# Performance work log

Measured on AMD Instinct MI355X. Metric: run time of the kernel, lower is better.

The kernel has to match this reference:

```python
import jax, jax.numpy as jnp
import numpy as np

B, N, S, D, K = 8, 8192, 2048, 256, 3
MLP = [256, 128]
EPS = 1e-5


def setup_inputs() -> dict:
    key = jax.random.key(0)
    ks = jax.random.split(key, 12)
    inp = {
        "xyz1": jax.random.normal(ks[0], (B, N, 3), dtype=jnp.float32),
        "xyz2": jax.random.normal(ks[1], (B, S, 3), dtype=jnp.float32),
        "points1": jax.random.normal(ks[2], (B, N, D), dtype=jnp.float32),
        "points2": jax.random.normal(ks[3], (B, S, D), dtype=jnp.float32),
        # relation conv: Conv2d(4 -> 1, kernel 1x1) == linear over last dim
        "rel_w": jax.random.normal(ks[4], (4,), dtype=jnp.float32) * 0.5,
        "rel_b": jnp.zeros((), dtype=jnp.float32),
        # mlp layer 0: Conv1d(2D -> 256, k=1) + BN
        "W0": jax.random.normal(ks[5], (MLP[0], 2 * D), dtype=jnp.float32) * (1.0 / np.sqrt(2 * D)),
        "b0": jnp.zeros((MLP[0],), dtype=jnp.float32),
        "g0": jnp.ones((MLP[0],), dtype=jnp.float32),
        "be0": jnp.zeros((MLP[0],), dtype=jnp.float32),
        # mlp layer 1: Conv1d(256 -> 128, k=1) + BN
        "W1": jax.random.normal(ks[6], (MLP[1], MLP[0]), dtype=jnp.float32) * (1.0 / np.sqrt(MLP[0])),
        "b1": jnp.zeros((MLP[1],), dtype=jnp.float32),
        "g1": jnp.ones((MLP[1],), dtype=jnp.float32),
        "be1": jnp.zeros((MLP[1],), dtype=jnp.float32),
    }
    return inp


def _gather(points, idx):
    # points: [B,S,C], idx: [B,N,K] -> [B,N,K,C]
    return jax.vmap(lambda p, i: p[i])(points, idx)


def _bn_relu(x, gamma, beta):
    # training-mode BatchNorm1d over [B,N,C]: stats over (B,N), biased var
    mean = jnp.mean(x, axis=(0, 1))
    var = jnp.var(x, axis=(0, 1))
    xn = (x - mean) * jax.lax.rsqrt(var + EPS)
    return jax.nn.relu(xn * gamma + beta)


def reference(xyz1, xyz2, points1, points2, rel_w, rel_b,
              W0, b0, g0, be0, W1, b1, g1, be1):
    # pairwise squared distances [B,N,S]
    d = (jnp.sum(xyz1 ** 2, -1)[:, :, None]
         + jnp.sum(xyz2 ** 2, -1)[:, None, :]
         - 2.0 * jnp.einsum('bnc,bmc->bnm', xyz1, xyz2))
    neg_d, idx = jax.lax.top_k(-d, K)          # K smallest distances
    dists = -neg_d                              # [B,N,K]

    offset = xyz1[:, :, None, :] - _gather(xyz2, idx)        # [B,N,K,3]
    rel = jnp.concatenate([dists[..., None], offset], -1)    # [B,N,K,4]
    weight = jax.nn.sigmoid(rel @ rel_w + rel_b)              # [B,N,K]

    interp = jnp.mean(_gather(points2, idx) * weight[..., None], axis=2)  # [B,N,D]
    h = jnp.concatenate([points1, interp], axis=-1)           # [B,N,2D]

    h = _bn_relu(jnp.einsum('bnc,oc->bno', h, W0) + b0, g0, be0)
    h = _bn_relu(jnp.einsum('bnc,oc->bno', h, W1) + b1, g1, be1)
    return h  # [B,N,128]
```

## Files before the change

kernel.cpp:

```cpp
#include <hip/hip_runtime.h>
#include <stdint.h>
#include <stddef.h>

#define B_   8
#define N_   8192
#define S_   2048
#define D_   256
#define M_   (B_*N_)
#define C0_  256
#define C1_  128
#define K2D_ 512
#define TS8_ 8
#define SEG8_ (S_/TS8_)
#define SWP_ 264

typedef __attribute__((ext_vector_type(8))) short short8;
typedef __attribute__((ext_vector_type(4))) float f32x4;
typedef __attribute__((ext_vector_type(2))) float f32x2;

__device__ __forceinline__ short f2bf(float f) {
  unsigned u = __float_as_uint(f);
  u += 0x7fffu + ((u >> 16) & 1u);
  return (short)(u >> 16);
}
__device__ __forceinline__ float bf2f(short s) {
  return __uint_as_float(((unsigned)(unsigned short)s) << 16);
}

__device__ __forceinline__ void cp16(const void* g, void* l) {
  __builtin_amdgcn_global_load_lds(
      (__attribute__((address_space(1))) void*)(g),
      (__attribute__((address_space(3))) void*)(l), 16, 0, 0);
}

__global__ void convw_kernel(const float* __restrict__ W0,
                             const float* __restrict__ W1,
                             const float* __restrict__ xyz2,
                             short* __restrict__ W0b, short* __restrict__ W1b,
                             float* __restrict__ xyz2p, float* __restrict__ stats) {
  int i = blockIdx.x * 256 + threadIdx.x;
  if (blockIdx.x == 0) {
    stats[threadIdx.x] = 0.f;
    stats[256 + threadIdx.x] = 0.f;
    stats[512 + threadIdx.x] = 0.f;
  }
  if (i < C0_ * K2D_) W0b[i] = f2bf(W0[i]);
  if (i < C1_ * C0_)  W1b[i] = f2bf(W1[i]);
  if (i < B_ * S_) {
    const int b = i >> 11, s = i & (S_ - 1);
    float x = xyz2[(size_t)i * 3 + 0];
    float y = xyz2[(size_t)i * 3 + 1];
    float z = xyz2[(size_t)i * 3 + 2];
    float ss = __fadd_rn(__fadd_rn(__fmul_rn(x, x), __fmul_rn(y, y)), __fmul_rn(z, z));
    float* xw = xyz2p + (size_t)b * 4 * S_;
    xw[s] = x; xw[S_ + s] = y; xw[2 * S_ + s] = z; xw[3 * S_ + s] = ss;
  }
}

__global__ __launch_bounds__(512, 8)
void topk_kernel(const float* __restrict__ xyz1, const float* __restrict__ xyz2p,
                 const float* __restrict__ relw, const float* __restrict__ relb,
                 int* __restrict__ idx_out, float* __restrict__ w_out) {
  __shared__ float cd[TS8_][64][3];
  __shared__ int   ci[TS8_][64][3];
  const int tid  = threadIdx.x;
  const int lane = tid & 63;
  const int seg  = __builtin_amdgcn_readfirstlane(tid >> 6);
  const int b    = blockIdx.x >> 7;
  const int n    = (blockIdx.x & 127) * 64 + lane;

  const float* p = xyz1 + ((size_t)b * N_ + n) * 3;
  const float ax = p[0], ay = p[1], az = p[2];
  const float s1 = __fadd_rn(__fadd_rn(__fmul_rn(ax, ax), __fmul_rn(ay, ay)), __fmul_rn(az, az));

  const float* xw = xyz2p + (size_t)b * 4 * S_;
  const f32x2* XP = (const f32x2*)(xw)           + seg * (SEG8_ / 2);
  const f32x2* YP = (const f32x2*)(xw + S_)      + seg * (SEG8_ / 2);
  const f32x2* ZP = (const f32x2*)(xw + 2 * S_)  + seg * (SEG8_ / 2);
  const f32x2* WP = (const f32x2*)(xw + 3 * S_)  + seg * (SEG8_ / 2);

  float d0 = 3.4e38f, d1 = 3.4e38f, d2 = 3.4e38f;
  int   i0 = 0, i1 = 0, i2 = 0;
  const int sbeg = seg * SEG8_;
  {
    #pragma clang fp contract(off)
    #pragma unroll 4
    for (int pr = 0; pr < SEG8_ / 2; pr++) {
      f32x2 X = XP[pr], Y = YP[pr], Z = ZP[pr], W = WP[pr];
      f32x2 t1 = ax * X;
      f32x2 t2 = ay * Y;
      f32x2 t3 = az * Z;
      f32x2 dt = (t1 + t2) + t3;
      f32x2 e  = s1 + W;
      f32x2 m  = 2.0f * dt;
      f32x2 d  = e - m;
      const float dlo = d.x, dhi = d.y;
      if (fminf(dlo, dhi) < d2) {
        const int s = sbeg + 2 * pr;
        if (dlo < d2) {
          if (dlo < d1) {
            d2 = d1; i2 = i1;
            if (dlo < d0) { d1 = d0; i1 = i0; d0 = dlo; i0 = s; }
            else          { d1 = dlo; i1 = s; }
          } else { d2 = dlo; i2 = s; }
        }
        if (dhi < d2) {
          if (dhi < d1) {
            d2 = d1; i2 = i1;
            if (dhi < d0) { d1 = d0; i1 = i0; d0 = dhi; i0 = s + 1; }
            else          { d1 = dhi; i1 = s + 1; }
          } else { d2 = dhi; i2 = s + 1; }
        }
      }
    }
  }
  cd[seg][lane][0] = d0; cd[seg][lane][1] = d1; cd[seg][lane][2] = d2;
  ci[seg][lane][0] = i0; ci[seg][lane][1] = i1; ci[seg][lane][2] = i2;
  __syncthreads();

  if (tid < 64) {
    float m0 = 3.4e38f, m1 = 3.4e38f, m2 = 3.4e38f;
    int   j0 = 0, j1 = 0, j2 = 0;
    #pragma unroll
    for (int sg = 0; sg < TS8_; sg++) {
      #pragma unroll
      for (int k = 0; k < 3; k++) {
        float d = cd[sg][tid][k];
        int   ix = ci[sg][tid][k];
        if (d < m2) {
          if (d < m1) {
            m2 = m1; j2 = j1;
            if (d < m0) { m1 = m0; j1 = j0; m0 = d; j0 = ix; }
            else        { m1 = d;  j1 = ix; }
          } else { m2 = d; j2 = ix; }
        }
      }
    }
    const float w0r = relw[0], w1r = relw[1], w2r = relw[2], w3r = relw[3], br = relb[0];
    const size_t base = ((size_t)b * N_ + n) * 3;
    float dd[3] = {m0, m1, m2};
    int   ii[3] = {j0, j1, j2};
    #pragma unroll
    for (int k = 0; k < 3; k++) {
      const int s = ii[k];
      float ox = ax - xw[s], oy = ay - xw[S_ + s], oz = az - xw[2 * S_ + s];
      float t = dd[k] * w0r + ox * w1r + oy * w2r + oz * w3r + br;
      float w = 1.0f / (1.0f + expf(-t));
      idx_out[base + k] = s;
      w_out[base + k] = w * (1.0f / 3.0f);
    }
  }
}

__global__ __launch_bounds__(256, 8)
void interp_kernel(const float* __restrict__ p1, const float* __restrict__ p2,
                   const int* __restrict__ idx, const float* __restrict__ wts,
                   short* __restrict__ h) {
  const int tid = threadIdx.x;
  const int seg = tid & 63;
  const size_t row = (size_t)(blockIdx.x & 7) * (M_ / 8)
                   + (size_t)(blockIdx.x >> 3) * 4 + (tid >> 6);
  short8 o;
  if (seg < 32) {
    const float* src = p1 + row * D_ + seg * 8;
    const float4 a = *(const float4*)src;
    const float4 b = *(const float4*)(src + 4);
    o[0] = f2bf(a.x); o[1] = f2bf(a.y); o[2] = f2bf(a.z); o[3] = f2bf(a.w);
    o[4] = f2bf(b.x); o[5] = f2bf(b.y); o[6] = f2bf(b.z); o[7] = f2bf(b.w);
    *(short8*)&h[row * K2D_ + seg * 8] = o;
  } else {
    const int c = (seg - 32) * 8;
    const int i0 = idx[row * 3 + 0], i1 = idx[row * 3 + 1], i2 = idx[row * 3 + 2];
    const float w0 = wts[row * 3 + 0], w1 = wts[row * 3 + 1], w2 = wts[row * 3 + 2];
    const float* pb = p2 + (row >> 13) * ((size_t)S_ * D_) + c;
    const float* q0 = pb + (size_t)i0 * D_;
    const float* q1 = pb + (size_t)i1 * D_;
    const float* q2 = pb + (size_t)i2 * D_;
    const float4 a0 = *(const float4*)q0, b0 = *(const float4*)(q0 + 4);
    const float4 a1 = *(const float4*)q1, b1 = *(const float4*)(q1 + 4);
    const float4 a2 = *(const float4*)q2, b2 = *(const float4*)(q2 + 4);
    float fv[8];
    fv[0] = w0 * a0.x + w1 * a1.x + w2 * a2.x;
    fv[1] = w0 * a0.y + w1 * a1.y + w2 * a2.y;
    fv[2] = w0 * a0.z + w1 * a1.z + w2 * a2.z;
    fv[3] = w0 * a0.w + w1 * a1.w + w2 * a2.w;
    fv[4] = w0 * b0.x + w1 * b1.x + w2 * b2.x;
    fv[5] = w0 * b0.y + w1 * b1.y + w2 * b2.y;
    fv[6] = w0 * b0.z + w1 * b1.z + w2 * b2.z;
    fv[7] = w0 * b0.w + w1 * b1.w + w2 * b2.w;
    #pragma unroll
    for (int e = 0; e < 8; e++) o[e] = f2bf(fv[e]);
    *(short8*)&h[row * K2D_ + D_ + c] = o;
  }
}

__global__ __launch_bounds__(256, 2)
void gemm1_kernel(const short* __restrict__ h, const short* __restrict__ Bw,
                  const float* __restrict__ bias,
                  short* __restrict__ Cb, float* __restrict__ stats) {
  __shared__ __align__(16) short sA[2][128 * 32];
  __shared__ __align__(16) short sB[2][256 * 32];
  const int tid = threadIdx.x;
  const int lane = tid & 63;
  const int wave = tid >> 6;
  const int wm = wave & 1;
  const int wn = wave >> 1;
  const size_t mbase = (size_t)(blockIdx.x & 7) * (M_ / 8)
                     + (size_t)(blockIdx.x >> 3) * 128;

  #define STAGE(K0, BUF)                                                      \
    _Pragma("unroll")                                                         \
    for (int t = 0; t < 2; t++) {                                             \
      const int ca = wave * 128 + t * 64 + lane;                              \
      cp16(h + (mbase + (ca >> 2)) * K2D_ + (K0) + (ca & 3) * 8,              \
           &sA[BUF][(wave * 128 + t * 64) * 8]);                              \
    }                                                                         \
    _Pragma("unroll")                                                         \
    for (int t = 0; t < 4; t++) {                                             \
      const int cb = wave * 256 + t * 64 + lane;                              \
      cp16(Bw + (size_t)(cb >> 2) * K2D_ + (K0) + (cb & 3) * 8,               \
           &sB[BUF][(wave * 256 + t * 64) * 8]);                              \
    }

  f32x4 acc[4][8] = {};
  STAGE(0, 0);

  const int mr = lane & 15;
  const int ks = (lane >> 4) * 8;

  for (int k0 = 0, it = 0; k0 < K2D_; k0 += 32, it++) {
    __syncthreads();
    const int kn = k0 + 32;
    if (kn < K2D_) STAGE(kn, (it + 1) & 1);

    short8 af[4], bfr[8];
    #pragma unroll
    for (int i = 0; i < 4; i++)
      af[i]  = *(const short8*)&sA[it & 1][(wm * 64 + i * 16 + mr) * 32 + ks];
    #pragma unroll
    for (int j = 0; j < 8; j++)
      bfr[j] = *(const short8*)&sB[it & 1][(wn * 128 + j * 16 + mr) * 32 + ks];
    #pragma unroll
    for (int i = 0; i < 4; i++)
      #pragma unroll
      for (int j = 0; j < 8; j++)
        acc[i][j] = __builtin_amdgcn_mfma_f32_16x16x32_bf16(af[i], bfr[j], acc[i][j], 0, 0, 0);
  }
  #undef STAGE
  __syncthreads();

  const int cr = (lane >> 4) * 4;
  const int cc = lane & 15;
  float ps[8], ps2[8];
  #pragma unroll
  for (int j = 0; j < 8; j++) {
    const int col = wn * 128 + j * 16 + cc;
    const float bv = bias[col];
    float s = 0.f, s2 = 0.f;
    #pragma unroll
    for (int i = 0; i < 4; i++) {
      #pragma unroll
      for (int r = 0; r < 4; r++) {
        const float vv = acc[i][j][r];
        s += vv; s2 += vv * vv;
        const size_t row = mbase + wm * 64 + i * 16 + cr + r;
        Cb[row * C0_ + col] = f2bf(vv + bv);
      }
    }
    ps[j] = s; ps2[j] = s2;
  }
  #pragma unroll
  for (int j = 0; j < 8; j++) {
    ps[j]  += __shfl_xor(ps[j], 16);  ps[j]  += __shfl_xor(ps[j], 32);
    ps2[j] += __shfl_xor(ps2[j], 16); ps2[j] += __shfl_xor(ps2[j], 32);
  }
  float* sred = (float*)sA;
  if (wm == 1 && lane < 16) {
    #pragma unroll
    for (int j = 0; j < 8; j++) {
      const int c = wn * 128 + j * 16 + lane;
      sred[2 * c] = ps[j]; sred[2 * c + 1] = ps2[j];
    }
  }
  __syncthreads();
  if (wm == 0 && lane < 16) {
    #pragma unroll
    for (int j = 0; j < 8; j++) {
      const int c = wn * 128 + j * 16 + lane;
      atomicAdd(&stats[c],       ps[j]  + sred[2 * c]);
      atomicAdd(&stats[C0_ + c], ps2[j] + sred[2 * c + 1]);
    }
  }
}

__global__ __launch_bounds__(256, 2)
void gemm2_kernel(const short* __restrict__ A, const short* __restrict__ Bw,
                  const float* __restrict__ ssn, const float* __restrict__ bias,
                  short* __restrict__ Cb, float* __restrict__ stats) {
  __shared__ __align__(16) short sW[C1_ * SWP_];
  __shared__ float sred[3 * 256];
  const int tid = threadIdx.x;
  const int lane = tid & 63;
  const int wave = tid >> 6;
  const size_t mbase = (size_t)blockIdx.x * 128;

  #pragma unroll
  for (int i = 0; i < 16; i++) {
    const int flat = i * 256 + tid;
    const int n = flat >> 5;
    const int kb = flat & 31;
    *(short8*)&sW[n * SWP_ + kb * 8] = *(const short8*)(Bw + (size_t)flat * 8);
  }
  __syncthreads();

  f32x4 acc[2][8] = {};
  const int mr = lane & 15;
  const int ksq = (lane >> 4) * 8;

  for (int k0 = 0; k0 < C0_; k0 += 32) {
    const int kk = k0 + ksq;
    float4 sc0 = *(const float4*)(ssn + kk);
    float4 sc1 = *(const float4*)(ssn + kk + 4);
    float4 sh0 = *(const float4*)(ssn + C0_ + kk);
    float4 sh1 = *(const float4*)(ssn + C0_ + kk + 4);
    const float sc[8] = {sc0.x, sc0.y, sc0.z, sc0.w, sc1.x, sc1.y, sc1.z, sc1.w};
    const float sh[8] = {sh0.x, sh0.y, sh0.z, sh0.w, sh1.x, sh1.y, sh1.z, sh1.w};
    short8 af[2];
    #pragma unroll
    for (int i = 0; i < 2; i++) {
      const size_t row = mbase + wave * 32 + i * 16 + mr;
      short8 av = *(const short8*)(A + row * C0_ + kk);
      short8 o;
      #pragma unroll
      for (int e = 0; e < 8; e++) {
        float f = bf2f(av[e]) * sc[e] + sh[e];
        o[e] = f2bf(f > 0.f ? f : 0.f);
      }
      af[i] = o;
    }
    short8 bf8[8];
    #pragma unroll
    for (int j = 0; j < 8; j++) bf8[j] = *(const short8*)&sW[(j * 16 + mr) * SWP_ + kk];
    #pragma unroll
    for (int i = 0; i < 2; i++)
      #pragma unroll
      for (int j = 0; j < 8; j++)
        acc[i][j] = __builtin_amdgcn_mfma_f32_16x16x32_bf16(af[i], bf8[j], acc[i][j], 0, 0, 0);
  }

  const int cr = (lane >> 4) * 4;
  const int cc = lane & 15;
  float ps[8], ps2[8];
  #pragma unroll
  for (int j = 0; j < 8; j++) {
    const int col = j * 16 + cc;
    const float bv = bias[col];
    float s = 0.f, s2 = 0.f;
    #pragma unroll
    for (int i = 0; i < 2; i++) {
      #pragma unroll
      for (int r = 0; r < 4; r++) {
        const float vv = acc[i][j][r];
        s += vv; s2 += vv * vv;
        const size_t row = mbase + wave * 32 + i * 16 + cr + r;
        Cb[row * C1_ + col] = f2bf(vv + bv);
      }
    }
    ps[j] = s; ps2[j] = s2;
  }
  #pragma unroll
  for (int j = 0; j < 8; j++) {
    ps[j]  += __shfl_xor(ps[j], 16);  ps[j]  += __shfl_xor(ps[j], 32);
    ps2[j] += __shfl_xor(ps2[j], 16); ps2[j] += __shfl_xor(ps2[j], 32);
  }
  if (wave > 0 && lane < 16) {
    #pragma unroll
    for (int j = 0; j < 8; j++) {
      const int c = j * 16 + lane;
      sred[(wave - 1) * 256 + c]       = ps[j];
      sred[(wave - 1) * 256 + 128 + c] = ps2[j];
    }
  }
  __syncthreads();
  if (wave == 0 && lane < 16) {
    #pragma unroll
    for (int j = 0; j < 8; j++) {
      const int c = j * 16 + lane;
      float s  = ps[j]  + sred[c]       + sred[256 + c]       + sred[512 + c];
      float s2 = ps2[j] + sred[128 + c] + sred[256 + 128 + c] + sred[512 + 128 + c];
      atomicAdd(&stats[c],       s);
      atomicAdd(&stats[C1_ + c], s2);
    }
  }
}

__global__ void stats_final_kernel(const float* __restrict__ stats, const int C,
                                   const float* __restrict__ bias,
                                   const float* __restrict__ g, const float* __restrict__ be,
                                   float* __restrict__ ss) {
  const int c = threadIdx.x;
  if (c >= C) return;
  const float inv = 1.0f / (float)M_;
  float m0 = stats[c] * inv;
  float var = stats[C + c] * inv - m0 * m0;
  float mean = m0 + bias[c];
  float sc = g[c] * rsqrtf(var + 1e-5f);
  ss[c] = sc;
  ss[C + c] = be[c] - mean * sc;
}

__global__ __launch_bounds__(256, 1)
void norm2_kernel(const short* __restrict__ a2, const float* __restrict__ ss,
                  float* __restrict__ out) {
  const size_t t = (size_t)blockIdx.x * 256 + threadIdx.x;
  const size_t base = t * 8;
  const int c = (int)(base & (C1_ - 1));
  short8 v8 = *(const short8*)(a2 + base);
  float vv[8];
  #pragma unroll
  for (int k = 0; k < 8; k++) {
    float v = bf2f(v8[k]) * ss[c + k] + ss[C1_ + c + k];
    vv[k] = v > 0.f ? v : 0.f;
  }
  *(float4*)(out + base)     = make_float4(vv[0], vv[1], vv[2], vv[3]);
  *(float4*)(out + base + 4) = make_float4(vv[4], vv[5], vv[6], vv[7]);
}

extern "C" void kernel_launch(void* const* d_in, const int* in_sizes, int n_in,
                              void* d_out, int out_size, void* d_ws, size_t ws_size,
                              hipStream_t stream) {
  const float* xyz1 = (const float*)d_in[0];
  const float* xyz2 = (const float*)d_in[1];
  const float* pts1 = (const float*)d_in[2];
  const float* pts2 = (const float*)d_in[3];
  const float* relw = (const float*)d_in[4];
  const float* relb = (const float*)d_in[5];
  const float* W0   = (const float*)d_in[6];
  const float* b0   = (const float*)d_in[7];
  const float* g0   = (const float*)d_in[8];
  const float* be0  = (const float*)d_in[9];
  const float* W1   = (const float*)d_in[10];
  const float* b1   = (const float*)d_in[11];
  const float* g1   = (const float*)d_in[12];
  const float* be1  = (const float*)d_in[13];

  char* ws = (char*)d_ws;
  constexpr size_t IDX_OFF = 0;
  constexpr size_t WTS_OFF = IDX_OFF + (size_t)M_ * 3 * 4;
  constexpr size_t W0B_OFF = WTS_OFF + (size_t)M_ * 3 * 4;
  constexpr size_t W1B_OFF = W0B_OFF + (size_t)C0_ * K2D_ * 2;
  constexpr size_t XW_OFF  = W1B_OFF + (size_t)C1_ * C0_ * 2;
  constexpr size_t H_OFF   = XW_OFF + (size_t)B_ * 4 * S_ * 4;
  constexpr size_t A1_OFF  = H_OFF + (size_t)M_ * K2D_ * 2;
  constexpr size_t A2_OFF  = A1_OFF + (size_t)M_ * C0_ * 2;
  constexpr size_t ST_OFF  = A2_OFF + (size_t)M_ * C1_ * 2;
  constexpr size_t SS1_OFF = ST_OFF + (size_t)768 * 4;
  constexpr size_t SS2_OFF = SS1_OFF + (size_t)2 * C0_ * 4;

  int*   idx   = (int*)(ws + IDX_OFF);
  float* wts   = (float*)(ws + WTS_OFF);
  short* W0b   = (short*)(ws + W0B_OFF);
  short* W1b   = (short*)(ws + W1B_OFF);
  float* xyz2p = (float*)(ws + XW_OFF);
  short* h     = (short*)(ws + H_OFF);
  short* a1    = (short*)(ws + A1_OFF);
  short* a2    = (short*)(ws + A2_OFF);
  float* st    = (float*)(ws + ST_OFF);
  float* ss1   = (float*)(ws + SS1_OFF);
  float* ss2   = (float*)(ws + SS2_OFF);
  float* outp  = (float*)d_out;

  convw_kernel<<<512, 256, 0, stream>>>(W0, W1, xyz2, W0b, W1b, xyz2p, st);
  topk_kernel<<<B_ * (N_ / 64), 512, 0, stream>>>(xyz1, xyz2p, relw, relb, idx, wts);

  interp_kernel<<<M_ * 64 / 256, 256, 0, stream>>>(pts1, pts2, idx, wts, h);
  gemm1_kernel<<<M_ / 128, 256, 0, stream>>>(h, W0b, b0, a1, st);
  stats_final_kernel<<<1, 256, 0, stream>>>(st, C0_, b0, g0, be0, ss1);

  gemm2_kernel<<<M_ / 128, 256, 0, stream>>>(a1, W1b, ss1, b1, a2, st + 512);
  stats_final_kernel<<<1, 128, 0, stream>>>(st + 512, C1_, b1, g1, be1, ss2);
  norm2_kernel<<<(size_t)M_ * C1_ / 8 / 256, 256, 0, stream>>>(a2, ss2, outp);
}
```

Baseline: 320.1 us.

## Fuse points1 bf16 conversion into gemm1 A staging and branchless top-3 insert

The points1 half of the concatenated activation is no longer written to a bf16 scratch buffer by interp_kernel. gemm1 now loads it directly as fp32, converts it to bf16 and stores it into LDS for the first half of K, and uses async LDS copies only for the interpolated half. This removes a write and a read of 32 MB of intermediate traffic, but the first-half A loads go through registers instead of global_load_lds, so less of the load overlaps with compute. Separately, the top-3 insertion in topk is made branchless using med3/min and selects, which removes divergence but executes the update for every candidate.

```diff
diff --git a/kernel.cpp b/kernel.cpp
--- a/kernel.cpp
+++ b/kernel.cpp
@@ -32,6 +32,19 @@
       (__attribute__((address_space(1))) void*)(g),
       (__attribute__((address_space(3))) void*)(l), 16, 0, 0);
 }
+
+#define INS3(v, si)                                                           \
+  {                                                                           \
+    const float v_ = (v); const int s_ = (si);                                \
+    const bool b0 = v_ < d0, b1 = v_ < d1, b2 = v_ < d2;                      \
+    const int   ni2 = b1 ? i1 : (b2 ? s_ : i2);                               \
+    const float nd2 = __builtin_amdgcn_fmed3f(v_, d1, d2);                    \
+    const int   ni1 = b0 ? i0 : (b1 ? s_ : i1);                               \
+    const float nd1 = __builtin_amdgcn_fmed3f(v_, d0, d1);                    \
+    const int   ni0 = b0 ? s_ : i0;                                           \
+    const float nd0 = fminf(v_, d0);                                          \
+    d0 = nd0; d1 = nd1; d2 = nd2; i0 = ni0; i1 = ni1; i2 = ni2;               \
+  }
 
 __global__ void convw_kernel(const float* __restrict__ W0,
                              const float* __restrict__ W1,
@@ -95,23 +108,9 @@
       f32x2 m  = 2.0f * dt;
       f32x2 d  = e - m;
       const float dlo = d.x, dhi = d.y;
-      if (fminf(dlo, dhi) < d2) {
-        const int s = sbeg + 2 * pr;
-        if (dlo < d2) {
-          if (dlo < d1) {
-            d2 = d1; i2 = i1;
-            if (dlo < d0) { d1 = d0; i1 = i0; d0 = dlo; i0 = s; }
-            else          { d1 = dlo; i1 = s; }
-          } else { d2 = dlo; i2 = s; }
-        }
-        if (dhi < d2) {
-          if (dhi < d1) {
-            d2 = d1; i2 = i1;
-            if (dhi < d0) { d1 = d0; i1 = i0; d0 = dhi; i0 = s + 1; }
-            else          { d1 = dhi; i1 = s + 1; }
-          } else { d2 = dhi; i2 = s + 1; }
-        }
-      }
+      const int s = sbeg + 2 * pr;
+      INS3(dlo, s);
+      INS3(dhi, s + 1);
     }
   }
   cd[seg][lane][0] = d0; cd[seg][lane][1] = d1; cd[seg][lane][2] = d2;
@@ -119,27 +118,21 @@
   __syncthreads();
 
   if (tid < 64) {
-    float m0 = 3.4e38f, m1 = 3.4e38f, m2 = 3.4e38f;
-    int   j0 = 0, j1 = 0, j2 = 0;
+    float d0 = 3.4e38f, d1 = 3.4e38f, d2 = 3.4e38f;
+    int   i0 = 0, i1 = 0, i2 = 0;
     #pragma unroll
     for (int sg = 0; sg < TS8_; sg++) {
       #pragma unroll
       for (int k = 0; k < 3; k++) {
-        float d = cd[sg][tid][k];
-        int   ix = ci[sg][tid][k];
-        if (d < m2) {
-          if (d < m1) {
-            m2 = m1; j2 = j1;
-            if (d < m0) { m1 = m0; j1 = j0; m0 = d; j0 = ix; }
-            else        { m1 = d;  j1 = ix; }
-          } else { m2 = d; j2 = ix; }
-        }
+        const float dv = cd[sg][tid][k];
+        const int   iv = ci[sg][tid][k];
+        INS3(dv, iv);
       }
     }
     const float w0r = relw[0], w1r = relw[1], w2r = relw[2], w3r = relw[3], br = relb[0];
     const size_t base = ((size_t)b * N_ + n) * 3;
-    float dd[3] = {m0, m1, m2};
-    int   ii[3] = {j0, j1, j2};
+    float dd[3] = {d0, d1, d2};
+    int   ii[3] = {i0, i1, i2};
     #pragma unroll
     for (int k = 0; k < 3; k++) {
       const int s = ii[k];
@@ -153,50 +146,39 @@
 }
 
 __global__ __launch_bounds__(256, 8)
-void interp_kernel(const float* __restrict__ p1, const float* __restrict__ p2,
-                   const int* __restrict__ idx, const float* __restrict__ wts,
-                   short* __restrict__ h) {
+void interp_kernel(const float* __restrict__ p2, const int* __restrict__ idx,
+                   const float* __restrict__ wts, short* __restrict__ hi) {
   const int tid = threadIdx.x;
-  const int seg = tid & 63;
-  const size_t row = (size_t)(blockIdx.x & 7) * (M_ / 8)
-                   + (size_t)(blockIdx.x >> 3) * 4 + (tid >> 6);
+  const size_t row = (size_t)(blockIdx.x & 7) * N_
+                   + (size_t)(blockIdx.x >> 3) * 8 + (tid >> 5);
+  const int c = (tid & 31) * 8;
+  const int j0 = idx[row * 3 + 0], j1 = idx[row * 3 + 1], j2 = idx[row * 3 + 2];
+  const float w0 = wts[row * 3 + 0], w1 = wts[row * 3 + 1], w2 = wts[row * 3 + 2];
+  const float* pb = p2 + (row >> 13) * ((size_t)S_ * D_) + c;
+  const float* q0 = pb + (size_t)j0 * D_;
+  const float* q1 = pb + (size_t)j1 * D_;
+  const float* q2 = pb + (size_t)j2 * D_;
+  const float4 a0 = *(const float4*)q0, b0 = *(const float4*)(q0 + 4);
+  const float4 a1 = *(const float4*)q1, b1 = *(const float4*)(q1 + 4);
+  const float4 a2 = *(const float4*)q2, b2 = *(const float4*)(q2 + 4);
+  float fv[8];
+  fv[0] = w0 * a0.x + w1 * a1.x + w2 * a2.x;
+  fv[1] = w0 * a0.y + w1 * a1.y + w2 * a2.y;
+  fv[2] = w0 * a0.z + w1 * a1.z + w2 * a2.z;
+  fv[3] = w0 * a0.w + w1 * a1.w + w2 * a2.w;
+  fv[4] = w0 * b0.x + w1 * b1.x + w2 * b2.x;
+  fv[5] = w0 * b0.y + w1 * b1.y + w2 * b2.y;
+  fv[6] = w0 * b0.z + w1 * b1.z + w2 * b2.z;
+  fv[7] = w0 * b0.w + w1 * b1.w + w2 * b2.w;
   short8 o;
-  if (seg < 32) {
-    const float* src = p1 + row * D_ + seg * 8;
-    const float4 a = *(const float4*)src;
-    const float4 b = *(const float4*)(src + 4);
-    o[0] = f2bf(a.x); o[1] = f2bf(a.y); o[2] = f2bf(a.z); o[3] = f2bf(a.w);
-    o[4] = f2bf(b.x); o[5] = f2bf(b.y); o[6] = f2bf(b.z); o[7] = f2bf(b.w);
-    *(short8*)&h[row * K2D_ + seg * 8] = o;
-  } else {
-    const int c = (seg - 32) * 8;
-    const int i0 = idx[row * 3 + 0], i1 = idx[row * 3 + 1], i2 = idx[row * 3 + 2];
-    const float w0 = wts[row * 3 + 0], w1 = wts[row * 3 + 1], w2 = wts[row * 3 + 2];
-    const float* pb = p2 + (row >> 13) * ((size_t)S_ * D_) + c;
-    const float* q0 = pb + (size_t)i0 * D_;
-    const float* q1 = pb + (size_t)i1 * D_;
-    const float* q2 = pb + (size_t)i2 * D_;
-    const float4 a0 = *(const float4*)q0, b0 = *(const float4*)(q0 + 4);
-    const float4 a1 = *(const float4*)q1, b1 = *(const float4*)(q1 + 4);
-    const float4 a2 = *(const float4*)q2, b2 = *(const float4*)(q2 + 4);
-    float fv[8];
-    fv[0] = w0 * a0.x + w1 * a1.x + w2 * a2.x;
-    fv[1] = w0 * a0.y + w1 * a1.y + w2 * a2.y;
-    fv[2] = w0 * a0.z + w1 * a1.z + w2 * a2.z;
-    fv[3] = w0 * a0.w + w1 * a1.w + w2 * a2.w;
-    fv[4] = w0 * b0.x + w1 * b1.x + w2 * b2.x;
-    fv[5] = w0 * b0.y + w1 * b1.y + w2 * b2.y;
-    fv[6] = w0 * b0.z + w1 * b1.z + w2 * b2.z;
-    fv[7] = w0 * b0.w + w1 * b1.w + w2 * b2.w;
-    #pragma unroll
-    for (int e = 0; e < 8; e++) o[e] = f2bf(fv[e]);
-    *(short8*)&h[row * K2D_ + D_ + c] = o;
-  }
+  #pragma unroll
+  for (int e = 0; e < 8; e++) o[e] = f2bf(fv[e]);
+  *(short8*)&hi[row * D_ + c] = o;
 }
 
 __global__ __launch_bounds__(256, 2)
-void gemm1_kernel(const short* __restrict__ h, const short* __restrict__ Bw,
-                  const float* __restrict__ bias,
+void gemm1_kernel(const float* __restrict__ p1, const short* __restrict__ hi,
+                  const short* __restrict__ Bw, const float* __restrict__ bias,
                   short* __restrict__ Cb, float* __restrict__ stats) {
   __shared__ __align__(16) short sA[2][128 * 32];
   __shared__ __align__(16) short sB[2][256 * 32];
@@ -205,16 +187,34 @@
   const int wave = tid >> 6;
   const int wm = wave & 1;
   const int wn = wave >> 1;
-  const size_t mbase = (size_t)(blockIdx.x & 7) * (M_ / 8)
+  const size_t mbase = (size_t)(blockIdx.x & 7) * N_
                      + (size_t)(blockIdx.x >> 3) * 128;
 
-  #define STAGE(K0, BUF)                                                      \
-    _Pragma("unroll")                                                         \
-    for (int t = 0; t < 2; t++) {                                             \
-      const int ca = wave * 128 + t * 64 + lane;                              \
-      cp16(h + (mbase + (ca >> 2)) * K2D_ + (K0) + (ca & 3) * 8,              \
-           &sA[BUF][(wave * 128 + t * 64) * 8]);                              \
-    }                                                                         \
+  #define STAGE_A(K0, BUF)                                                    \
+    if ((K0) < D_) {                                                          \
+      _Pragma("unroll")                                                       \
+      for (int t = 0; t < 2; t++) {                                           \
+        const int c = tid * 2 + t;                                            \
+        const int r = c >> 2; const int sc = (c & 3) * 8;                     \
+        const float* src = p1 + (mbase + r) * D_ + (K0) + sc;                 \
+        const float4 va = *(const float4*)src;                                \
+        const float4 vb = *(const float4*)(src + 4);                          \
+        short8 o;                                                             \
+        o[0] = f2bf(va.x); o[1] = f2bf(va.y); o[2] = f2bf(va.z);              \
+        o[3] = f2bf(va.w); o[4] = f2bf(vb.x); o[5] = f2bf(vb.y);              \
+        o[6] = f2bf(vb.z); o[7] = f2bf(vb.w);                                 \
+        *(short8*)&sA[BUF][r * 32 + sc] = o;                                  \
+      }                                                                       \
+    } else {                                                                  \
+      _Pragma("unroll")                                                       \
+      for (int t = 0; t < 2; t++) {                                           \
+        const int ca = wave * 128 + t * 64 + lane;                            \
+        cp16(hi + (mbase + (ca >> 2)) * D_ + ((K0) - D_) + (ca & 3) * 8,      \
+             &sA[BUF][(wave * 128 + t * 64) * 8]);                            \
+      }                                                                       \
+    }
+
+  #define STAGE_B(K0, BUF)                                                    \
     _Pragma("unroll")                                                         \
     for (int t = 0; t < 4; t++) {                                             \
       const int cb = wave * 256 + t * 64 + lane;                              \
@@ -223,7 +223,8 @@
     }
 
   f32x4 acc[4][8] = {};
-  STAGE(0, 0);
+  STAGE_A(0, 0);
+  STAGE_B(0, 0);
 
   const int mr = lane & 15;
   const int ks = (lane >> 4) * 8;
@@ -231,7 +232,10 @@
   for (int k0 = 0, it = 0; k0 < K2D_; k0 += 32, it++) {
     __syncthreads();
     const int kn = k0 + 32;
-    if (kn < K2D_) STAGE(kn, (it + 1) & 1);
+    if (kn < K2D_) {
+      STAGE_A(kn, (it + 1) & 1);
+      STAGE_B(kn, (it + 1) & 1);
+    }
 
     short8 af[4], bfr[8];
     #pragma unroll
@@ -246,7 +250,8 @@
       for (int j = 0; j < 8; j++)
         acc[i][j] = __builtin_amdgcn_mfma_f32_16x16x32_bf16(af[i], bfr[j], acc[i][j], 0, 0, 0);
   }
-  #undef STAGE
+  #undef STAGE_A
+  #undef STAGE_B
   __syncthreads();
 
   const int cr = (lane >> 4) * 4;
@@ -450,8 +455,8 @@
   constexpr size_t W0B_OFF = WTS_OFF + (size_t)M_ * 3 * 4;
   constexpr size_t W1B_OFF = W0B_OFF + (size_t)C0_ * K2D_ * 2;
   constexpr size_t XW_OFF  = W1B_OFF + (size_t)C1_ * C0_ * 2;
-  constexpr size_t H_OFF   = XW_OFF + (size_t)B_ * 4 * S_ * 4;
-  constexpr size_t A1_OFF  = H_OFF + (size_t)M_ * K2D_ * 2;
+  constexpr size_t HI_OFF  = XW_OFF + (size_t)B_ * 4 * S_ * 4;
+  constexpr size_t A1_OFF  = HI_OFF + (size_t)M_ * D_ * 2;
   constexpr size_t A2_OFF  = A1_OFF + (size_t)M_ * C0_ * 2;
   constexpr size_t ST_OFF  = A2_OFF + (size_t)M_ * C1_ * 2;
   constexpr size_t SS1_OFF = ST_OFF + (size_t)768 * 4;
@@ -462,7 +467,7 @@
   short* W0b   = (short*)(ws + W0B_OFF);
   short* W1b   = (short*)(ws + W1B_OFF);
   float* xyz2p = (float*)(ws + XW_OFF);
-  short* h     = (short*)(ws + H_OFF);
+  short* hi    = (short*)(ws + HI_OFF);
   short* a1    = (short*)(ws + A1_OFF);
   short* a2    = (short*)(ws + A2_OFF);
   float* st    = (float*)(ws + ST_OFF);
@@ -473,8 +478,8 @@
   convw_kernel<<<512, 256, 0, stream>>>(W0, W1, xyz2, W0b, W1b, xyz2p, st);
   topk_kernel<<<B_ * (N_ / 64), 512, 0, stream>>>(xyz1, xyz2p, relw, relb, idx, wts);
 
-  interp_kernel<<<M_ * 64 / 256, 256, 0, stream>>>(pts1, pts2, idx, wts, h);
-  gemm1_kernel<<<M_ / 128, 256, 0, stream>>>(h, W0b, b0, a1, st);
+  interp_kernel<<<M_ * 32 / 256, 256, 0, stream>>>(pts2, idx, wts, hi);
+  gemm1_kernel<<<M_ / 128, 256, 0, stream>>>(pts1, hi, W0b, b0, a1, st);
   stats_final_kernel<<<1, 256, 0, stream>>>(st, C0_, b0, g0, be0, ss1);
 
   gemm2_kernel<<<M_ / 128, 256, 0, stream>>>(a1, W1b, ss1, b1, a2, st + 512);
```

Measured after the change: 287.6 us. 1.11x faster.
